# Kernel optimization log

Measured on AMD Instinct MI355X. Metric: run time of the kernel, lower is better.

## Reference

```python
import jax, jax.numpy as jnp
import numpy as np

H = W = 64
ALPHA = 1.0
BETA = 100.0
LIMB_PAIRS = np.array([[0,1],[1,2],[2,3],[0,4],[4,5],[5,6],[0,7],[7,8],[8,9],[9,10],
                       [8,11],[11,12],[12,13],[8,14],[14,15],[15,16]])
P0 = LIMB_PAIRS[:, 0]
P1 = LIMB_PAIRS[:, 1]
_last = {}
for _l, _j in enumerate(P0):
    _last[int(_j)] = _l
J0 = np.array(list(_last.keys()))   # unique proximal joints
L0 = np.array(list(_last.values())) # last limb writing to each joint


def make_kernel(h, w, alpha):
    # replicates: coords = stack(meshgrid(arange(2h-1), arange(2w-1))).transpose(1,2) (h==w)
    ii, jj = jnp.meshgrid(jnp.arange(2 * h - 1), jnp.arange(2 * w - 1), indexing='ij')
    ker = jnp.stack([h - jj, w - ii], axis=0).astype(jnp.float32)  # (2, 2h-1, 2w-1)
    dist = jnp.linalg.norm(ker, axis=0, keepdims=True)
    dist = dist.at[0, h, w].set(1.0)
    return ker / dist ** (1.0 + alpha)


def corr_full(x, k):
    # x: (N, Cin, h, w); k: (Cout, Cin, 2h-1, 2w-1); 'same' correlation with pad h-1/w-1
    h, w = x.shape[-2:]
    return jax.lax.conv_general_dilated(x, k, (1, 1), ((h - 1, h - 1), (w - 1, w - 1)))


def heatmap_std(x, di=False):
    axes = (3, 4, 5) if di else (3, 4)
    return jnp.std(x, axis=axes, keepdims=True, ddof=1)


def heatmap_normalize(x, std, di=False):
    return x * std / (heatmap_std(x, di) + 1e-6)


def l2norm(v, axis):
    return v / jnp.maximum(jnp.linalg.norm(v, axis=axis, keepdims=True), 1e-12)


def soft_argmax(hm, beta):
    # hm: ... x h x w -> ... x 2 with (row_coord, col_coord) as in the torch code
    h, w = hm.shape[-2:]
    p = jax.nn.softmax(hm.reshape(hm.shape[:-2] + (-1,)) * beta, axis=-1).reshape(hm.shape)
    rows = jnp.arange(h, dtype=p.dtype)[:, None]
    cols = jnp.arange(w, dtype=p.dtype)[None, :]
    norm = p.sum((-2, -1))
    kp_x = (p * rows).sum((-2, -1)) / norm
    kp_y = (p * cols).sum((-2, -1)) / norm
    return jnp.stack((kp_x, kp_y), axis=-1)


def scale_pts(pts, image_shape, h, w):
    return jnp.stack((pts[..., 0] * image_shape[1] / w,
                      pts[..., 1] * image_shape[0] / h), axis=-1)


def cofix_forward(heatmaps, fields, Ps, Rs, Cs, image_shape, confs, vth1, vth2, pth1, pth2):
    bs, nv, nL, _, h, w = fields.shape
    nJ = heatmaps.shape[2]
    K = make_kernel(h, w, ALPHA)  # (2, 2h-1, 2w-1)

    heatmaps = heatmaps - jnp.mean(heatmaps, axis=(3, 4), keepdims=True)
    std_hm = heatmap_std(heatmaps, di=False)
    std_df = heatmap_std(fields, di=True)

    Hs = heatmaps[:, :, P1] - heatmaps[:, :, P0]  # (bs, nv, nL, h, w)
    # conv3d(kernel1, flipped Hs) == 'same' correlation of Hs with spatially-reversed K
    k1 = K[:, ::-1, ::-1][:, None]  # (2, 1, 2h-1, 2w-1)
    convs = corr_full(Hs.reshape(-1, 1, h, w), k1).reshape(bs, nv, nL, 2, h, w)

    coef = jax.nn.relu(jnp.sum(convs * fields[..., :2, :, :], axis=3, keepdims=True))
    fields_new = fields * coef

    fnorm = jnp.linalg.norm(fields, axis=3, keepdims=True)
    lvecs = l2norm(jnp.sum(fnorm * fields, axis=(4, 5)), axis=3)
    lpts = scale_pts(soft_argmax(fnorm[:, :, :, 0], BETA), image_shape, h, w)

    fnorm_new = jnp.linalg.norm(fields_new, axis=3, keepdims=True)
    lvecs_new = l2norm(jnp.sum(fnorm_new * fields_new, axis=(4, 5)), axis=3)
    lpts_new = scale_pts(soft_argmax(fnorm_new[:, :, :, 0], BETA), image_shape, h, w)

    # original code computes vec_selection(...) then overwrites: delta[:] = 0
    delta = jnp.zeros((bs, nv, nL, 1), dtype=heatmaps.dtype)
    comb_v = delta * lvecs_new + (1 - delta) * lvecs
    comb_p = delta * lpts_new + (1 - delta) * lpts

    d6 = delta[..., None, None]
    fields_c = heatmap_normalize(fields * (1 - d6) + fields_new * d6, std_df, di=True)

    # conv2d(kernel2, fields) then output spatial flip == 'same' correlation with K
    k2 = K[None]  # (1, 2, 2h-1, 2w-1)
    fds2jts = corr_full(fields_c[..., :2, :, :].reshape(-1, 2, h, w), k2)
    fds2jts = fds2jts.reshape(bs, nv, nL, h, w)
    prox_ = jax.nn.relu(-fds2jts)
    dist_ = jax.nn.relu(fds2jts)

    hms_new = heatmaps.at[:, :, J0].set(heatmaps[:, :, J0] * prox_[:, :, L0])
    hms_new = hms_new.at[:, :, P1].set(hms_new[:, :, P1] * dist_)
    hms_new = heatmap_normalize(hms_new, std_hm, di=False)

    kps = scale_pts(soft_argmax(heatmaps, BETA), image_shape, h, w)[..., None]
    kps_new = scale_pts(soft_argmax(hms_new, BETA), image_shape, h, w)[..., None]
    kps_new = jnp.where(jnp.isnan(kps_new), kps, kps_new)

    # sed_selection (reconstructed): keep refined kps where joint conf is high and
    # the refinement displacement is small.
    confs_j = confs[:, :, nL:]
    disp = jnp.linalg.norm((kps_new - kps)[..., 0], axis=-1)  # (bs, nv, nJ)
    sel = ((confs_j > pth1) & (disp < pth2)).astype(kps.dtype)[..., None, None]
    kps_combined = sel * kps_new + (1 - sel) * kps

    return kps_combined, comb_v, comb_p, fields_new, hms_new


def setup_inputs() -> dict:
    key = jax.random.key(0)
    ks = jax.random.split(key, 6)
    bs, nv, nJ, nL = 4, 4, 17, 16
    return {
        'heatmaps': jax.random.uniform(ks[0], (bs, nv, nJ, H, W), jnp.float32),
        'fields': jax.random.normal(ks[1], (bs, nv, nL, 3, H, W), jnp.float32),
        'Ps': jax.random.normal(ks[2], (bs, nv, 3, 4), jnp.float32),
        'Rs': jax.random.normal(ks[3], (bs, nv, 3, 3), jnp.float32),
        'Cs': jax.random.normal(ks[4], (bs, nv, 3, 1), jnp.float32),
        'image_shape': jnp.array([384, 384], jnp.int32),
        'confs': jax.random.uniform(ks[5], (bs, nv, nL + nJ), jnp.float32),
        'vth1': 0.5, 'vth2': 0.5, 'pth1': 0.1, 'pth2': 20.0,
    }


def reference(heatmaps, fields, Ps, Rs, Cs, image_shape, confs, vth1, vth2, pth1, pth2):
    return cofix_forward(heatmaps, fields, Ps, Rs, Cs, image_shape, confs,
                         vth1, vth2, pth1, pth2)
```

## Files before the change

### kernel.cpp

```cpp
#include <hip/hip_runtime.h>
#include <math.h>

#define TPB 1024
#define HTPB 256
#define NPIX 4096
#define NJ 17
#define NL 16
static constexpr float kBeta = 100.0f;

#define O_KPS 0
#define O_CV 544
#define O_CP 1312
#define O_FN 1824
#define O_HM 3147552
#define W_FDS 0
#define W_MEAN 1048576
#define W_STD 1048848
#define W_SF 1049120
#define W_W1 1049376
#define W_W2 1082144

__device__ __constant__ int c_P0[16] = {0,1,2,0,4,5,0,7,8,9,8,11,12,8,14,15};
__device__ __constant__ int c_P1[16] = {1,2,3,4,5,6,7,8,9,10,11,12,13,14,15,16};
__device__ __constant__ int c_proxL[17] = {6,1,2,-1,4,5,-1,7,13,9,-1,11,12,-1,14,15,-1};
__device__ __constant__ int c_distL[17] = {-1,0,1,2,3,4,5,6,7,8,9,10,11,12,13,14,15};

using cplx = float2;
__device__ inline cplx cadd(cplx a, cplx b){ return {a.x+b.x, a.y+b.y}; }
__device__ inline cplx csub(cplx a, cplx b){ return {a.x-b.x, a.y-b.y}; }
__device__ inline cplx cmul(cplx a, cplx w){ return {a.x*w.x - a.y*w.y, a.x*w.y + a.y*w.x}; }
__device__ inline cplx cmulc(cplx a, cplx w){ return {a.x*w.x + a.y*w.y, a.y*w.x - a.x*w.y}; }

template<bool ROWS> __device__ inline int AD(int line, int p){
  return ROWS ? ((line<<7) | (p ^ (line & 15))) : ((p<<7) | (line ^ (p & 15)));
}

template<bool ROWS, bool INV, bool ZTOP, int NL_>
__device__ void pass_r2(cplx* S, const cplx* TW, int tid){
  constexpr int LOG2 = (NL_==128)?7:6;
  const int total = NL_*64;
  for (int idx = tid; idx < total; idx += TPB){
    const int line = idx & (NL_-1);
    const int b = idx >> LOG2;
    const cplx w = TW[b];
    const int a0 = AD<ROWS>(line, b);
    const int a1 = AD<ROWS>(line, b+64);
    if (ZTOP){
      const cplx u = S[a0];
      S[a1] = cmul(u, w);
    } else if (!INV){
      const cplx u = S[a0], v = S[a1];
      S[a0] = cadd(u,v);
      S[a1] = cmul(csub(u,v), w);
    } else {
      const cplx u = S[a0], t = cmulc(S[a1], w);
      S[a0] = cadd(u,t);
      S[a1] = csub(u,t);
    }
  }
  __syncthreads();
}

template<bool ROWS, bool INV, int Q, int NL_>
__device__ void pass_r4(cplx* S, const cplx* TW, int tid){
  constexpr int LOG2 = (NL_==128)?7:6;
  constexpr int LQ = (Q==16)?4:((Q==4)?2:0);
  constexpr int S_ = 32/Q;
  const int total = NL_*32;
  for (int idx = tid; idx < total; idx += TPB){
    const int line = idx & (NL_-1);
    const int b = idx >> LOG2;
    const int j = b & (Q-1);
    const int blk = b >> LQ;
    const int p0 = blk*(4*Q) + j;
    const int a0 = AD<ROWS>(line, p0);
    const int a1 = AD<ROWS>(line, p0+Q);
    const int a2 = AD<ROWS>(line, p0+2*Q);
    const int a3 = AD<ROWS>(line, p0+3*Q);
    const cplx x0=S[a0], x1=S[a1], x2=S[a2], x3=S[a3];
    if constexpr (!INV){
      const cplx a = cadd(x0,x2), bb = csub(x0,x2);
      const cplx c = cadd(x1,x3), d = csub(x1,x3);
      const cplx dp = {d.y, -d.x};
      if constexpr (Q==1){
        S[a0] = cadd(a,c);  S[a1] = csub(a,c);
        S[a2] = cadd(bb,dp); S[a3] = csub(bb,dp);
      } else {
        const cplx w1 = TW[j*S_], w2 = TW[2*j*S_], w3 = TW[3*j*S_];
        S[a0] = cadd(a,c);
        S[a1] = cmul(csub(a,c), w2);
        S[a2] = cmul(cadd(bb,dp), w1);
        S[a3] = cmul(csub(bb,dp), w3);
      }
    } else {
      cplx z1, z2, z3;
      if constexpr (Q==1){ z1 = x1; z2 = x2; z3 = x3; }
      else {
        const cplx w1 = TW[j*S_], w2 = TW[2*j*S_], w3 = TW[3*j*S_];
        z1 = cmulc(x1,w2); z2 = cmulc(x2,w1); z3 = cmulc(x3,w3);
      }
      const cplx A = cadd(x0,z1), C = csub(x0,z1);
      const cplx B = cadd(z2,z3), D = csub(z2,z3);
      const cplx iD = {-D.y, D.x};
      S[a0] = cadd(A,B);
      S[a1] = cadd(C,iD);
      S[a2] = csub(A,B);
      S[a3] = csub(C,iD);
    }
  }
  __syncthreads();
}

__device__ inline void tw_init(cplx* TW, int tid){
  if (tid < 96){
    float s, c;
    sincosf(-3.14159265358979323846f * (float)tid / 64.0f, &s, &c);
    TW[tid] = {c, s};
  }
  __syncthreads();
}

__device__ inline void fft2d_fwd_conv(cplx* S, const cplx* TW, int tid){
  pass_r2<true,  false, true, 64 >(S, TW, tid);
  pass_r4<true,  false, 16,   64 >(S, TW, tid);
  pass_r4<true,  false, 4,    64 >(S, TW, tid);
  pass_r4<true,  false, 1,    64 >(S, TW, tid);
  pass_r2<false, false, true, 128>(S, TW, tid);
  pass_r4<false, false, 16,   128>(S, TW, tid);
  pass_r4<false, false, 4,    128>(S, TW, tid);
  pass_r4<false, false, 1,    128>(S, TW, tid);
}
__device__ inline void fft2d_inv_conv(cplx* S, const cplx* TW, int tid){
  pass_r4<false, true, 1,    128>(S, TW, tid);
  pass_r4<false, true, 4,    128>(S, TW, tid);
  pass_r4<false, true, 16,   128>(S, TW, tid);
  pass_r2<false, true, false,128>(S, TW, tid);
  pass_r4<true,  true, 1,    64 >(S, TW, tid);
  pass_r4<true,  true, 4,    64 >(S, TW, tid);
  pass_r4<true,  true, 16,   64 >(S, TW, tid);
  pass_r2<true,  true, false,64 >(S, TW, tid);
}
__device__ inline void fft2d_fwd_full(cplx* S, const cplx* TW, int tid){
  pass_r2<true,  false, false,128>(S, TW, tid);
  pass_r4<true,  false, 16,   128>(S, TW, tid);
  pass_r4<true,  false, 4,    128>(S, TW, tid);
  pass_r4<true,  false, 1,    128>(S, TW, tid);
  pass_r2<false, false, false,128>(S, TW, tid);
  pass_r4<false, false, 16,   128>(S, TW, tid);
  pass_r4<false, false, 4,    128>(S, TW, tid);
  pass_r4<false, false, 1,    128>(S, TW, tid);
}

template<int N>
__device__ inline void reduce3n(float& a, float& b, float& c,
                                float* s0, float* s1, float* s2, int tid){
  s0[tid]=a; s1[tid]=b; s2[tid]=c; __syncthreads();
  for (int st = N/2; st; st >>= 1){
    if (tid < st){ s0[tid]+=s0[tid+st]; s1[tid]+=s1[tid+st]; s2[tid]+=s2[tid+st]; }
    __syncthreads();
  }
  a=s0[0]; b=s1[0]; c=s2[0]; __syncthreads();
}
template<int N>
__device__ inline float reduce_maxn(float v, float* s0, int tid){
  s0[tid]=v; __syncthreads();
  for (int st = N/2; st; st >>= 1){
    if (tid < st) s0[tid] = fmaxf(s0[tid], s0[tid+st]);
    __syncthreads();
  }
  const float r = s0[0]; __syncthreads();
  return r;
}

__global__ __launch_bounds__(TPB,1) void pre_kernel(const float* __restrict__ heat,
                                                    const float* __restrict__ fields,
                                                    const int* __restrict__ ishape,
                                                    float* __restrict__ mean_hm,
                                                    float* __restrict__ std_hm,
                                                    float* __restrict__ sf,
                                                    float* __restrict__ W1,
                                                    float* __restrict__ W2,
                                                    float* __restrict__ out){
  __shared__ cplx S[16384];
  __shared__ cplx TW[96];
  __shared__ float sA[TPB], sB[TPB], sC[TPB];
  const int tid = threadIdx.x;
  const int blk = blockIdx.x;
  if (blk < 272){
    const float* p = heat + (size_t)blk * NPIX;
    float s = 0.0f, s2 = 0.0f, d = 0.0f;
    for (int i = 0; i < 4; i++){
      const float x = p[tid + i*TPB];
      s += x; s2 += x*x;
    }
    reduce3n<TPB>(s, s2, d, sA, sB, sC, tid);
    if (tid == 0){
      const float mean = s / 4096.0f;
      const float var = (s2 - s*mean) / 4095.0f;
      mean_hm[blk] = mean;
      std_hm[blk] = sqrtf(fmaxf(var, 0.0f));
    }
  } else if (blk < 528){
    const int m = blk - 272;
    const float* f = fields + (size_t)m * 3 * NPIX;
    float s1 = 0.0f, s2 = 0.0f;
    float a0 = 0.0f, a1 = 0.0f, a2 = 0.0f;
    float fn[4];
    for (int i = 0; i < 4; i++){
      const int px = tid + i*TPB;
      const float f0 = f[px], f1 = f[NPIX+px], f2 = f[2*NPIX+px];
      s1 += f0+f1+f2; s2 += f0*f0+f1*f1+f2*f2;
      const float nn = sqrtf(f0*f0 + f1*f1 + f2*f2);
      fn[i] = nn;
      a0 += nn*f0; a1 += nn*f1; a2 += nn*f2;
    }
    {
      float t1 = s1, t2 = s2, t3 = 0.0f;
      reduce3n<TPB>(t1, t2, t3, sA, sB, sC, tid);
      if (tid == 0){
        const float var = (t2 - t1*t1/12288.0f) / 12287.0f;
        const float sd = sqrtf(fmaxf(var, 0.0f));
        sf[m] = sd / (sd + 1e-6f);
      }
    }
    reduce3n<TPB>(a0, a1, a2, sA, sB, sC, tid);
    float mx = fmaxf(fmaxf(fn[0],fn[1]), fmaxf(fn[2],fn[3]));
    mx = reduce_maxn<TPB>(mx, sA, tid);
    float Sm = 0.0f, Sx = 0.0f, Sy = 0.0f;
    for (int i = 0; i < 4; i++){
      const int px = tid + i*TPB;
      const float e = expf(kBeta * (fn[i] - mx));
      Sm += e; Sx += e * (float)(px>>6); Sy += e * (float)(px&63);
    }
    reduce3n<TPB>(Sm, Sx, Sy, sA, sB, sC, tid);
    if (tid == 0){
      float nrm = sqrtf(a0*a0 + a1*a1 + a2*a2);
      nrm = fmaxf(nrm, 1e-12f);
      out[O_CV + m*3 + 0] = a0/nrm;
      out[O_CV + m*3 + 1] = a1/nrm;
      out[O_CV + m*3 + 2] = a2/nrm;
      const float sxs = (float)ishape[1] / 64.0f;
      const float sys = (float)ishape[0] / 64.0f;
      out[O_CP + m*2 + 0] = Sx/Sm * sxs;
      out[O_CP + m*2 + 1] = Sy/Sm * sys;
    }
  } else {
    const int which = blk - 528;
    tw_init(TW, tid);
    for (int i = tid; i < 16384; i += TPB){
      const int r = i >> 7, c = i & 127;
      const int dy = (r < 64) ? r : r - 128;
      const int dx = (c < 64) ? c : c - 128;
      float a, b;
      if (which == 0){ a = 1.0f - (float)dy; b = 1.0f - (float)dx; }
      else           { a = 1.0f + (float)dy; b = 1.0f + (float)dx; }
      const float den = a*a + b*b;
      float vr = 0.0f, vi = 0.0f;
      if (r != 64 && c != 64 && den > 0.0f){
        const float inv = 1.0f/den;
        vr = a*inv; vi = -b*inv;
      }
      S[(r<<7) | (c ^ (r & 15))] = {vr, vi};
    }
    __syncthreads();
    fft2d_fwd_full(S, TW, tid);
    float2* Wo = (float2*)((which == 0) ? W1 : W2);
    const float scl = 1.0f / 16384.0f;
    for (int i = tid; i < 16384; i += TPB) Wo[i] = {S[i].x*scl, S[i].y*scl};
  }
}

__global__ __launch_bounds__(TPB,1) void conv_kernel(const float* __restrict__ heat,
                                                     const float* __restrict__ mean_hm,
                                                     const float* __restrict__ fields,
                                                     const float* __restrict__ sf,
                                                     const float* __restrict__ W1g,
                                                     const float* __restrict__ W2g,
                                                     float* __restrict__ out_fn,
                                                     float* __restrict__ fds){
  __shared__ cplx S[16384];
  __shared__ cplx TW[96];
  const int tid = threadIdx.x;
  const int n = blockIdx.x;
  tw_init(TW, tid);
  if (n < 256){
    const int bv = n >> 4, l = n & 15;
    const int j1 = bv*NJ + c_P1[l], j0 = bv*NJ + c_P0[l];
    const float* h1 = heat + (size_t)j1 * NPIX;
    const float* h0 = heat + (size_t)j0 * NPIX;
    const float dm = mean_hm[j1] - mean_hm[j0];
    for (int i = tid; i < NPIX; i += TPB){
      const int y = i >> 6, x = i & 63;
      S[(y<<7) | (x ^ (y & 15))] = {h1[i] - h0[i] - dm, 0.0f};
    }
    __syncthreads();
    fft2d_fwd_conv(S, TW, tid);
    const float2* Wg = (const float2*)W1g;
    for (int i = tid; i < 16384; i += TPB) S[i] = cmul(S[i], Wg[i]);
    __syncthreads();
    fft2d_inv_conv(S, TW, tid);
    const float* f = fields + (size_t)n * 3 * NPIX;
    float* o = out_fn + (size_t)n * 3 * NPIX;
    for (int i = tid; i < NPIX; i += TPB){
      const int y = i >> 6, x = i & 63;
      const cplx v = S[(y<<7) | (x ^ (y & 15))];
      const float c1 = v.x, c0 = -v.y;
      const float f0 = f[i], f1 = f[NPIX+i], f2 = f[2*NPIX+i];
      const float coef = fmaxf(0.0f, c0*f0 + c1*f1);
      o[i] = f0*coef; o[NPIX+i] = f1*coef; o[2*NPIX+i] = f2*coef;
    }
  } else {
    const int m = n - 256;
    const float* f = fields + (size_t)m * 3 * NPIX;
    for (int i = tid; i < NPIX; i += TPB){
      const int y = i >> 6, x = i & 63;
      S[(y<<7) | (x ^ (y & 15))] = {f[NPIX+i], f[i]};
    }
    __syncthreads();
    fft2d_fwd_conv(S, TW, tid);
    const float2* Wg = (const float2*)W2g;
    for (int i = tid; i < 16384; i += TPB) S[i] = cmul(S[i], Wg[i]);
    __syncthreads();
    fft2d_inv_conv(S, TW, tid);
    const float s = sf[m];
    float* o = fds + (size_t)m * NPIX;
    for (int i = tid; i < NPIX; i += TPB){
      const int y = i >> 6, x = i & 63;
      o[i] = S[(y<<7) | (x ^ (y & 15))].x * s;
    }
  }
}

__global__ __launch_bounds__(HTPB) void hms_kernel(const float* __restrict__ heat,
                                                   const float* __restrict__ mean_hm,
                                                   const float* __restrict__ std_hm,
                                                   const float* __restrict__ fds,
                                                   const float* __restrict__ confs,
                                                   const int* __restrict__ ishape,
                                                   const float* __restrict__ pth1p,
                                                   const float* __restrict__ pth2p,
                                                   float* __restrict__ out){
  __shared__ float sA[HTPB], sB[HTPB], sC[HTPB];
  const int tid = threadIdx.x;
  const int idx = blockIdx.x;
  const int bv = idx / NJ, j = idx % NJ;
  const float* hp = heat + (size_t)idx * NPIX;
  const float mh = mean_hm[idx];
  const int pl = c_proxL[j], dl = c_distL[j];
  const float* fp = (pl >= 0) ? fds + (size_t)(bv*NL + pl) * NPIX : nullptr;
  const float* fd = (dl >= 0) ? fds + (size_t)(bv*NL + dl) * NPIX : nullptr;
  float ho[16], hn[16];
  float s = 0.0f, s2 = 0.0f, dummy = 0.0f;
  for (int i = 0; i < 16; i++){
    const int px = tid + i*HTPB;
    const float h = hp[px] - mh;
    ho[i] = h;
    float m = h;
    if (pl >= 0) m *= fmaxf(0.0f, -fp[px]);
    if (dl >= 0) m *= fmaxf(0.0f, fd[px]);
    hn[i] = m;
    s += m; s2 += m*m;
  }
  reduce3n<HTPB>(s, s2, dummy, sA, sB, sC, tid);
  const float var = (s2 - s*s/4096.0f) / 4095.0f;
  const float sdn = sqrtf(fmaxf(var, 0.0f));
  const float scale = std_hm[idx] / (sdn + 1e-6f);
  float* ohm = out + O_HM + (size_t)idx * NPIX;
  for (int i = 0; i < 16; i++){
    hn[i] *= scale;
    ohm[tid + i*HTPB] = hn[i];
  }
  float mo = -1e30f, mn = -1e30f;
  for (int i = 0; i < 16; i++){ mo = fmaxf(mo, ho[i]); mn = fmaxf(mn, hn[i]); }
  mo = reduce_maxn<HTPB>(mo, sA, tid);
  mn = reduce_maxn<HTPB>(mn, sA, tid);
  float So = 0.0f, Sxo = 0.0f, Syo = 0.0f;
  float Sn = 0.0f, Sxn = 0.0f, Syn = 0.0f;
  for (int i = 0; i < 16; i++){
    const int px = tid + i*HTPB;
    const float y = (float)(px >> 6), x = (float)(px & 63);
    const float eo = expf(kBeta * (ho[i] - mo));
    So += eo; Sxo += eo*y; Syo += eo*x;
    const float en = expf(kBeta * (hn[i] - mn));
    Sn += en; Sxn += en*y; Syn += en*x;
  }
  reduce3n<HTPB>(So, Sxo, Syo, sA, sB, sC, tid);
  reduce3n<HTPB>(Sn, Sxn, Syn, sA, sB, sC, tid);
  if (tid == 0){
    const float sxs = (float)ishape[1] / 64.0f;
    const float sys = (float)ishape[0] / 64.0f;
    const float kxo = Sxo/So * sxs, kyo = Syo/So * sys;
    float kxn = Sxn/Sn * sxs, kyn = Syn/Sn * sys;
    if (kxn != kxn) kxn = kxo;
    if (kyn != kyn) kyn = kyo;
    const float ddx = kxn - kxo, ddy = kyn - kyo;
    const float disp = sqrtf(ddx*ddx + ddy*ddy);
    const float conf = confs[bv*(NL+NJ) + NL + j];
    const bool sel = (conf > pth1p[0]) && (disp < pth2p[0]);
    out[O_KPS + idx*2 + 0] = sel ? kxn : kxo;
    out[O_KPS + idx*2 + 1] = sel ? kyn : kyo;
  }
}

extern "C" void kernel_launch(void* const* d_in, const int* in_sizes, int n_in,
                              void* d_out, int out_size, void* d_ws, size_t ws_size,
                              hipStream_t stream) {
  const float* heat   = (const float*)d_in[0];
  const float* fields = (const float*)d_in[1];
  const int*   ishape = (const int*)d_in[5];
  const float* confs  = (const float*)d_in[6];
  const float* pth1   = (const float*)d_in[9];
  const float* pth2   = (const float*)d_in[10];
  float* out = (float*)d_out;
  float* ws = (float*)d_ws;
  float* fds     = ws + W_FDS;
  float* mean_hm = ws + W_MEAN;
  float* std_hm  = ws + W_STD;
  float* sf      = ws + W_SF;
  float* W1      = ws + W_W1;
  float* W2      = ws + W_W2;

  hipLaunchKernelGGL(pre_kernel, dim3(530), dim3(TPB), 0, stream,
                     heat, fields, ishape, mean_hm, std_hm, sf, W1, W2, out);
  hipLaunchKernelGGL(conv_kernel, dim3(512), dim3(TPB), 0, stream,
                     heat, mean_hm, fields, sf, W1, W2, out + O_FN, fds);
  hipLaunchKernelGGL(hms_kernel, dim3(272), dim3(HTPB), 0, stream,
                     heat, mean_hm, std_hm, fds, confs, ishape, pth1, pth2, out);
}
```

Measured before the change: 174.3 us.

## Replace radix-2/4 shared-memory FFT passes with register radix-8x16 decomposition

Rewrites the 128x128 2D FFT convolution so each thread loads a column or row chunk into registers and runs radix-8 then radix-16 butterflies. This cuts the number of shared-memory passes and __syncthreads barriers from eight to about four per direction. The frequency-domain multiply is fused into the middle column stage, and storage uses float4 pairs with an XOR swizzle. Loads and stores are vectorised, and launch bounds are relaxed. The cost is more register pressure from the 16-element register arrays, plus a risk of indexing or twiddle errors in the new decomposition.

```diff
diff --git a/kernel.cpp b/kernel.cpp
--- a/kernel.cpp
+++ b/kernel.cpp
@@ -7,6 +7,7 @@
 #define NJ 17
 #define NL 16
 static constexpr float kBeta = 100.0f;
+static constexpr float S2H = 0.70710678118654752f;
 
 #define O_KPS 0
 #define O_CV 544
@@ -31,124 +32,265 @@
 __device__ inline cplx cmul(cplx a, cplx w){ return {a.x*w.x - a.y*w.y, a.x*w.y + a.y*w.x}; }
 __device__ inline cplx cmulc(cplx a, cplx w){ return {a.x*w.x + a.y*w.y, a.y*w.x - a.x*w.y}; }
 
-template<bool ROWS> __device__ inline int AD(int line, int p){
-  return ROWS ? ((line<<7) | (p ^ (line & 15))) : ((p<<7) | (line ^ (p & 15)));
-}
-
-template<bool ROWS, bool INV, bool ZTOP, int NL_>
-__device__ void pass_r2(cplx* S, const cplx* TW, int tid){
-  constexpr int LOG2 = (NL_==128)?7:6;
-  const int total = NL_*64;
-  for (int idx = tid; idx < total; idx += TPB){
-    const int line = idx & (NL_-1);
-    const int b = idx >> LOG2;
-    const cplx w = TW[b];
-    const int a0 = AD<ROWS>(line, b);
-    const int a1 = AD<ROWS>(line, b+64);
-    if (ZTOP){
-      const cplx u = S[a0];
-      S[a1] = cmul(u, w);
-    } else if (!INV){
-      const cplx u = S[a0], v = S[a1];
-      S[a0] = cadd(u,v);
-      S[a1] = cmul(csub(u,v), w);
-    } else {
-      const cplx u = S[a0], t = cmulc(S[a1], w);
-      S[a0] = cadd(u,t);
-      S[a1] = csub(u,t);
-    }
-  }
-  __syncthreads();
-}
-
-template<bool ROWS, bool INV, int Q, int NL_>
-__device__ void pass_r4(cplx* S, const cplx* TW, int tid){
-  constexpr int LOG2 = (NL_==128)?7:6;
-  constexpr int LQ = (Q==16)?4:((Q==4)?2:0);
-  constexpr int S_ = 32/Q;
-  const int total = NL_*32;
-  for (int idx = tid; idx < total; idx += TPB){
-    const int line = idx & (NL_-1);
-    const int b = idx >> LOG2;
-    const int j = b & (Q-1);
-    const int blk = b >> LQ;
-    const int p0 = blk*(4*Q) + j;
-    const int a0 = AD<ROWS>(line, p0);
-    const int a1 = AD<ROWS>(line, p0+Q);
-    const int a2 = AD<ROWS>(line, p0+2*Q);
-    const int a3 = AD<ROWS>(line, p0+3*Q);
-    const cplx x0=S[a0], x1=S[a1], x2=S[a2], x3=S[a3];
-    if constexpr (!INV){
-      const cplx a = cadd(x0,x2), bb = csub(x0,x2);
-      const cplx c = cadd(x1,x3), d = csub(x1,x3);
-      const cplx dp = {d.y, -d.x};
-      if constexpr (Q==1){
-        S[a0] = cadd(a,c);  S[a1] = csub(a,c);
-        S[a2] = cadd(bb,dp); S[a3] = csub(bb,dp);
-      } else {
-        const cplx w1 = TW[j*S_], w2 = TW[2*j*S_], w3 = TW[3*j*S_];
-        S[a0] = cadd(a,c);
-        S[a1] = cmul(csub(a,c), w2);
-        S[a2] = cmul(cadd(bb,dp), w1);
-        S[a3] = cmul(csub(bb,dp), w3);
-      }
-    } else {
-      cplx z1, z2, z3;
-      if constexpr (Q==1){ z1 = x1; z2 = x2; z3 = x3; }
-      else {
-        const cplx w1 = TW[j*S_], w2 = TW[2*j*S_], w3 = TW[3*j*S_];
-        z1 = cmulc(x1,w2); z2 = cmulc(x2,w1); z3 = cmulc(x3,w3);
-      }
-      const cplx A = cadd(x0,z1), C = csub(x0,z1);
-      const cplx B = cadd(z2,z3), D = csub(z2,z3);
-      const cplx iD = {-D.y, D.x};
-      S[a0] = cadd(A,B);
-      S[a1] = cadd(C,iD);
-      S[a2] = csub(A,B);
-      S[a3] = csub(C,iD);
-    }
-  }
-  __syncthreads();
-}
-
-__device__ inline void tw_init(cplx* TW, int tid){
-  if (tid < 96){
-    float s, c;
-    sincosf(-3.14159265358979323846f * (float)tid / 64.0f, &s, &c);
-    TW[tid] = {c, s};
-  }
-  __syncthreads();
-}
-
-__device__ inline void fft2d_fwd_conv(cplx* S, const cplx* TW, int tid){
-  pass_r2<true,  false, true, 64 >(S, TW, tid);
-  pass_r4<true,  false, 16,   64 >(S, TW, tid);
-  pass_r4<true,  false, 4,    64 >(S, TW, tid);
-  pass_r4<true,  false, 1,    64 >(S, TW, tid);
-  pass_r2<false, false, true, 128>(S, TW, tid);
-  pass_r4<false, false, 16,   128>(S, TW, tid);
-  pass_r4<false, false, 4,    128>(S, TW, tid);
-  pass_r4<false, false, 1,    128>(S, TW, tid);
-}
-__device__ inline void fft2d_inv_conv(cplx* S, const cplx* TW, int tid){
-  pass_r4<false, true, 1,    128>(S, TW, tid);
-  pass_r4<false, true, 4,    128>(S, TW, tid);
-  pass_r4<false, true, 16,   128>(S, TW, tid);
-  pass_r2<false, true, false,128>(S, TW, tid);
-  pass_r4<true,  true, 1,    64 >(S, TW, tid);
-  pass_r4<true,  true, 4,    64 >(S, TW, tid);
-  pass_r4<true,  true, 16,   64 >(S, TW, tid);
-  pass_r2<true,  true, false,64 >(S, TW, tid);
-}
-__device__ inline void fft2d_fwd_full(cplx* S, const cplx* TW, int tid){
-  pass_r2<true,  false, false,128>(S, TW, tid);
-  pass_r4<true,  false, 16,   128>(S, TW, tid);
-  pass_r4<true,  false, 4,    128>(S, TW, tid);
-  pass_r4<true,  false, 1,    128>(S, TW, tid);
-  pass_r2<false, false, false,128>(S, TW, tid);
-  pass_r4<false, false, 16,   128>(S, TW, tid);
-  pass_r4<false, false, 4,    128>(S, TW, tid);
-  pass_r4<false, false, 1,    128>(S, TW, tid);
+__device__ __constant__ float2 W128BR[8] = {
+  {1.f,0.f},
+  {0.98078528040323044913f,-0.19509032201612826785f},
+  {0.99518472667219688624f,-0.09801714032956060199f},
+  {0.95694033573220886494f,-0.29028467725446236764f},
+  {0.99879545620517239271f,-0.04906767432741801425f},
+  {0.97003125319454399260f,-0.24298017990326388995f},
+  {0.98917650996478097345f,-0.14673047445536175166f},
+  {0.94154406518302077841f,-0.33688985339222005069f}
+};
+__device__ __constant__ float2 W16BR[8] = {
+  {1.f,0.f},
+  {0.f,-1.f},
+  {0.70710678118654752440f,-0.70710678118654752440f},
+  {-0.70710678118654752440f,-0.70710678118654752440f},
+  {0.92387953251128675613f,-0.38268343236508977173f},
+  {-0.38268343236508977173f,-0.92387953251128675613f},
+  {0.38268343236508977173f,-0.92387953251128675613f},
+  {-0.92387953251128675613f,-0.38268343236508977173f}
+};
+
+__device__ inline void bf8_tail(cplx t0, cplx t1, cplx t2, cplx t3,
+                                cplx t4, cplx t5, cplx t6, cplx t7, cplx x[8]){
+  cplx u0=cadd(t0,t2), u2=csub(t0,t2);
+  cplx u1=cadd(t1,t3), d13=csub(t1,t3);
+  cplx u3={d13.y,-d13.x};
+  cplx u4=cadd(t4,t6), u6=csub(t4,t6);
+  cplx u5=cadd(t5,t7), d57=csub(t5,t7);
+  cplx u7={d57.y,-d57.x};
+  x[0]=cadd(u0,u1); x[1]=csub(u0,u1);
+  x[2]=cadd(u2,u3); x[3]=csub(u2,u3);
+  x[4]=cadd(u4,u5); x[5]=csub(u4,u5);
+  x[6]=cadd(u6,u7); x[7]=csub(u6,u7);
+}
+__device__ inline void bf8_fwd(cplx x[8]){
+  cplx t0=cadd(x[0],x[4]), d4=csub(x[0],x[4]);
+  cplx t1=cadd(x[1],x[5]), d5=csub(x[1],x[5]);
+  cplx t2=cadd(x[2],x[6]), d6=csub(x[2],x[6]);
+  cplx t3=cadd(x[3],x[7]), d7=csub(x[3],x[7]);
+  cplx t5={S2H*(d5.x+d5.y), S2H*(d5.y-d5.x)};
+  cplx t6={d6.y,-d6.x};
+  cplx t7={S2H*(d7.y-d7.x), -S2H*(d7.x+d7.y)};
+  bf8_tail(t0,t1,t2,t3,d4,t5,t6,t7,x);
+}
+__device__ inline void bf8_fwd_z(cplx x[8]){
+  cplx t5={S2H*(x[1].x+x[1].y), S2H*(x[1].y-x[1].x)};
+  cplx t6={x[2].y,-x[2].x};
+  cplx t7={S2H*(x[3].y-x[3].x), -S2H*(x[3].x+x[3].y)};
+  bf8_tail(x[0],x[1],x[2],x[3],x[0],t5,t6,t7,x);
+}
+__device__ inline void bf8_inv(cplx y[8]){
+  cplx u0=cadd(y[0],y[1]), u1=csub(y[0],y[1]);
+  cplx u2=cadd(y[2],y[3]), u3=csub(y[2],y[3]);
+  cplx u4=cadd(y[4],y[5]), u5=csub(y[4],y[5]);
+  cplx u6=cadd(y[6],y[7]), u7=csub(y[6],y[7]);
+  cplx t0=cadd(u0,u2), t2=csub(u0,u2);
+  cplx iu3={-u3.y,u3.x};
+  cplx t1=cadd(u1,iu3), t3=csub(u1,iu3);
+  cplx t4=cadd(u4,u6), t6=csub(u4,u6);
+  cplx iu7={-u7.y,u7.x};
+  cplx t5=cadd(u5,iu7), t7=csub(u5,iu7);
+  y[0]=cadd(t0,t4); y[4]=csub(t0,t4);
+  cplx w5={S2H*(t5.x-t5.y), S2H*(t5.x+t5.y)};
+  y[1]=cadd(t1,w5); y[5]=csub(t1,w5);
+  cplx w6={-t6.y,t6.x};
+  y[2]=cadd(t2,w6); y[6]=csub(t2,w6);
+  cplx w7={-S2H*(t7.x+t7.y), S2H*(t7.x-t7.y)};
+  y[3]=cadd(t3,w7); y[7]=csub(t3,w7);
+}
+
+__device__ inline void fft16_fwd(cplx z[16]){
+  cplx e[8], o[8];
+  #pragma unroll
+  for (int t=0;t<8;t++){ e[t]=z[2*t]; o[t]=z[2*t+1]; }
+  bf8_fwd(e); bf8_fwd(o);
+  #pragma unroll
+  for (int p=0;p<8;p++){
+    cplx vo = cmul(o[p], W16BR[p]);
+    z[2*p]   = cadd(e[p], vo);
+    z[2*p+1] = csub(e[p], vo);
+  }
+}
+__device__ inline void fft16_inv(cplx z[16]){
+  cplx e[8], o[8];
+  #pragma unroll
+  for (int p=0;p<8;p++){
+    cplx a=z[2*p], b=z[2*p+1];
+    e[p] = cadd(a,b);
+    o[p] = cmulc(csub(a,b), W16BR[p]);
+  }
+  bf8_inv(e); bf8_inv(o);
+  #pragma unroll
+  for (int t=0;t<8;t++){ z[2*t]=e[t]; z[2*t+1]=o[t]; }
+}
+
+__device__ inline void twchainA(const cplx* TW, int j, cplx A[8]){
+  cplx W1 = TW[j];
+  cplx W2 = cmul(W1,W1);
+  cplx W4 = cmul(W2,W2);
+  cplx W6 = cmul(W4,W2);
+  A[0] = {1.f,0.f}; A[1] = W4; A[2] = W2; A[3] = W6;
+  A[4] = W1; A[5] = cmul(W4,W1); A[6] = cmul(W2,W1); A[7] = cmul(W6,W1);
+}
+
+__device__ inline int PH(int y, int m){ return (y<<6) | ((m ^ ((y&7)*9)) & 63); }
+
+template<int NLINES, bool ZT>
+__device__ void row_s1_fwd(float4* S4, const cplx* TW, int tid){
+  if (tid < NLINES*8){
+    const int L = tid>>3, m = tid&7;
+    cplx xe[8], xo[8];
+    #pragma unroll
+    for (int t=0; t<(ZT?4:8); t++){
+      float4 v = S4[PH(L, m+8*t)];
+      xe[t]={v.x,v.y}; xo[t]={v.z,v.w};
+    }
+    if (ZT){ bf8_fwd_z(xe); bf8_fwd_z(xo); } else { bf8_fwd(xe); bf8_fwd(xo); }
+    cplx A[8]; twchainA(TW, 2*m, A);
+    #pragma unroll
+    for (int p=0;p<8;p++){
+      cplx B = cmul(A[p], W128BR[p]);
+      cplx ve = cmul(xe[p], A[p]);
+      cplx vo = cmul(xo[p], B);
+      S4[PH(L, m+8*p)] = {ve.x, ve.y, vo.x, vo.y};
+    }
+  }
+  __syncthreads();
+}
+__device__ void row_s1_inv(float4* S4, const cplx* TW, int tid){
+  if (tid < 512){
+    const int L = tid>>3, m = tid&7;
+    cplx xe[8], xo[8];
+    #pragma unroll
+    for (int p=0;p<8;p++){
+      float4 v = S4[PH(L, m+8*p)];
+      xe[p]={v.x,v.y}; xo[p]={v.z,v.w};
+    }
+    cplx A[8]; twchainA(TW, 2*m, A);
+    #pragma unroll
+    for (int p=0;p<8;p++){
+      cplx B = cmul(A[p], W128BR[p]);
+      xe[p] = cmulc(xe[p], A[p]);
+      xo[p] = cmulc(xo[p], B);
+    }
+    bf8_inv(xe); bf8_inv(xo);
+    #pragma unroll
+    for (int t=0;t<4;t++)
+      S4[PH(L, m+8*t)] = {xe[t].x, xe[t].y, xo[t].x, xo[t].y};
+  }
+  __syncthreads();
+}
+template<int NLINES>
+__device__ void row_s2_fwd(float4* S4, int tid){
+  if (tid < NLINES*8){
+    const int L = tid>>3, jb = tid&7;
+    cplx z[16];
+    #pragma unroll
+    for (int k=0;k<8;k++){
+      float4 v = S4[PH(L, jb*8+k)];
+      z[2*k]={v.x,v.y}; z[2*k+1]={v.z,v.w};
+    }
+    fft16_fwd(z);
+    #pragma unroll
+    for (int k=0;k<8;k++)
+      S4[PH(L, jb*8+k)] = {z[2*k].x, z[2*k].y, z[2*k+1].x, z[2*k+1].y};
+  }
+  __syncthreads();
+}
+__device__ void row_s2_inv(float4* S4, int tid){
+  if (tid < 512){
+    const int L = tid>>3, jb = tid&7;
+    cplx z[16];
+    #pragma unroll
+    for (int k=0;k<8;k++){
+      float4 v = S4[PH(L, jb*8+k)];
+      z[2*k]={v.x,v.y}; z[2*k+1]={v.z,v.w};
+    }
+    fft16_inv(z);
+    #pragma unroll
+    for (int k=0;k<8;k++)
+      S4[PH(L, jb*8+k)] = {z[2*k].x, z[2*k].y, z[2*k+1].x, z[2*k+1].y};
+  }
+  __syncthreads();
+}
+template<bool ZT>
+__device__ void col_s1_fwd(float4* S4, const cplx* TW, int tid){
+  const int cp = tid & 63, yj = tid >> 6;
+  const int sl = (cp ^ ((yj&7)*9)) & 63;
+  cplx xe[8], xo[8];
+  #pragma unroll
+  for (int t=0; t<(ZT?4:8); t++){
+    float4 v = S4[((yj+16*t)<<6) | sl];
+    xe[t]={v.x,v.y}; xo[t]={v.z,v.w};
+  }
+  if (ZT){ bf8_fwd_z(xe); bf8_fwd_z(xo); } else { bf8_fwd(xe); bf8_fwd(xo); }
+  cplx A[8]; twchainA(TW, yj, A);
+  #pragma unroll
+  for (int p=0;p<8;p++){
+    cplx ve = cmul(xe[p], A[p]);
+    cplx vo = cmul(xo[p], A[p]);
+    S4[((yj+16*p)<<6) | sl] = {ve.x, ve.y, vo.x, vo.y};
+  }
+  __syncthreads();
+}
+__device__ void col_s1_inv(float4* S4, const cplx* TW, int tid){
+  const int cp = tid & 63, yj = tid >> 6;
+  const int sl = (cp ^ ((yj&7)*9)) & 63;
+  cplx xe[8], xo[8];
+  #pragma unroll
+  for (int p=0;p<8;p++){
+    float4 v = S4[((yj+16*p)<<6) | sl];
+    xe[p]={v.x,v.y}; xo[p]={v.z,v.w};
+  }
+  cplx A[8]; twchainA(TW, yj, A);
+  #pragma unroll
+  for (int p=0;p<8;p++){
+    xe[p] = cmulc(xe[p], A[p]);
+    xo[p] = cmulc(xo[p], A[p]);
+  }
+  bf8_inv(xe); bf8_inv(xo);
+  #pragma unroll
+  for (int t=0;t<4;t++)
+    S4[((yj+16*t)<<6) | sl] = {xe[t].x, xe[t].y, xo[t].x, xo[t].y};
+  __syncthreads();
+}
+__device__ void col_s2_fused(float4* S4, const cplx* __restrict__ Wg, int tid){
+  cplx* Sc = (cplx*)S4;
+  const int c = tid & 127, r = tid >> 7;
+  const int ch = c & 1, cp = c >> 1;
+  int ad[16];
+  cplx z[16];
+  #pragma unroll
+  for (int i=0;i<16;i++){
+    const int y = 16*r + i;
+    ad[i] = ((((y<<6) | ((cp ^ ((y&7)*9)) & 63)) << 1) | ch);
+    z[i] = Sc[ad[i]];
+  }
+  fft16_fwd(z);
+  #pragma unroll
+  for (int i=0;i<16;i++) z[i] = cmul(z[i], Wg[(16*r+i)*128 + c]);
+  fft16_inv(z);
+  #pragma unroll
+  for (int i=0;i<16;i++) Sc[ad[i]] = z[i];
+  __syncthreads();
+}
+__device__ void col_s2_fwd_store(float4* S4, cplx* __restrict__ Wo, int tid){
+  cplx* Sc = (cplx*)S4;
+  const int c = tid & 127, r = tid >> 7;
+  const int ch = c & 1, cp = c >> 1;
+  cplx z[16];
+  #pragma unroll
+  for (int i=0;i<16;i++){
+    const int y = 16*r + i;
+    z[i] = Sc[(((y<<6) | ((cp ^ ((y&7)*9)) & 63)) << 1) | ch];
+  }
+  fft16_fwd(z);
+  const float scl = 1.0f / 16384.0f;
+  #pragma unroll
+  for (int i=0;i<16;i++) Wo[(16*r+i)*128 + c] = {z[i].x*scl, z[i].y*scl};
 }
 
 template<int N>
@@ -172,7 +314,19 @@
   return r;
 }
 
-__global__ __launch_bounds__(TPB,1) void pre_kernel(const float* __restrict__ heat,
+__device__ inline cplx wval(int r, int c, int which){
+  const int dy = (r<64)? r : r-128;
+  const int dx = (c<64)? c : c-128;
+  float a, b;
+  if (which==0){ a = 1.f-(float)dy; b = 1.f-(float)dx; }
+  else         { a = 1.f+(float)dy; b = 1.f+(float)dx; }
+  const float den = a*a + b*b;
+  if (r==64 || c==64 || den<=0.f) return {0.f,0.f};
+  const float inv = 1.f/den;
+  return {a*inv, -b*inv};
+}
+
+__global__ __launch_bounds__(TPB,4) void pre_kernel(const float* __restrict__ heat,
                                                     const float* __restrict__ fields,
                                                     const int* __restrict__ ishape,
                                                     float* __restrict__ mean_hm,
@@ -181,8 +335,8 @@
                                                     float* __restrict__ W1,
                                                     float* __restrict__ W2,
                                                     float* __restrict__ out){
-  __shared__ cplx S[16384];
-  __shared__ cplx TW[96];
+  __shared__ float4 S4[8192];
+  __shared__ cplx TW[128];
   __shared__ float sA[TPB], sB[TPB], sC[TPB];
   const int tid = threadIdx.x;
   const int blk = blockIdx.x;
@@ -246,31 +400,26 @@
     }
   } else {
     const int which = blk - 528;
-    tw_init(TW, tid);
-    for (int i = tid; i < 16384; i += TPB){
-      const int r = i >> 7, c = i & 127;
-      const int dy = (r < 64) ? r : r - 128;
-      const int dx = (c < 64) ? c : c - 128;
-      float a, b;
-      if (which == 0){ a = 1.0f - (float)dy; b = 1.0f - (float)dx; }
-      else           { a = 1.0f + (float)dy; b = 1.0f + (float)dx; }
-      const float den = a*a + b*b;
-      float vr = 0.0f, vi = 0.0f;
-      if (r != 64 && c != 64 && den > 0.0f){
-        const float inv = 1.0f/den;
-        vr = a*inv; vi = -b*inv;
-      }
-      S[(r<<7) | (c ^ (r & 15))] = {vr, vi};
+    if (tid < 128){
+      float s, c;
+      sincosf(-6.283185307179586f * (float)tid / 128.0f, &s, &c);
+      TW[tid] = {c, s};
+    }
+    for (int s = tid; s < 8192; s += TPB){
+      const int y = s>>6, m = s&63;
+      const cplx v0 = wval(y, 2*m, which);
+      const cplx v1 = wval(y, 2*m+1, which);
+      S4[PH(y, m)] = {v0.x, v0.y, v1.x, v1.y};
     }
     __syncthreads();
-    fft2d_fwd_full(S, TW, tid);
-    float2* Wo = (float2*)((which == 0) ? W1 : W2);
-    const float scl = 1.0f / 16384.0f;
-    for (int i = tid; i < 16384; i += TPB) Wo[i] = {S[i].x*scl, S[i].y*scl};
-  }
-}
-
-__global__ __launch_bounds__(TPB,1) void conv_kernel(const float* __restrict__ heat,
+    row_s1_fwd<128,false>(S4, TW, tid);
+    row_s2_fwd<128>(S4, tid);
+    col_s1_fwd<false>(S4, TW, tid);
+    col_s2_fwd_store(S4, (cplx*)((which==0)?W1:W2), tid);
+  }
+}
+
+__global__ __launch_bounds__(TPB,4) void conv_kernel(const float* __restrict__ heat,
                                                      const float* __restrict__ mean_hm,
                                                      const float* __restrict__ fields,
                                                      const float* __restrict__ sf,
@@ -278,55 +427,71 @@
                                                      const float* __restrict__ W2g,
                                                      float* __restrict__ out_fn,
                                                      float* __restrict__ fds){
-  __shared__ cplx S[16384];
-  __shared__ cplx TW[96];
+  __shared__ float4 S4[8192];
+  __shared__ cplx TW[128];
   const int tid = threadIdx.x;
   const int n = blockIdx.x;
-  tw_init(TW, tid);
-  if (n < 256){
+  const bool is1 = (n < 256);
+  const int m_img = is1 ? n : (n - 256);
+  if (tid < 128){
+    float s, c;
+    sincosf(-6.283185307179586f * (float)tid / 128.0f, &s, &c);
+    TW[tid] = {c, s};
+  }
+  const float* f = fields + (size_t)m_img * 3 * NPIX;
+  if (is1){
     const int bv = n >> 4, l = n & 15;
     const int j1 = bv*NJ + c_P1[l], j0 = bv*NJ + c_P0[l];
     const float* h1 = heat + (size_t)j1 * NPIX;
     const float* h0 = heat + (size_t)j0 * NPIX;
     const float dm = mean_hm[j1] - mean_hm[j0];
-    for (int i = tid; i < NPIX; i += TPB){
-      const int y = i >> 6, x = i & 63;
-      S[(y<<7) | (x ^ (y & 15))] = {h1[i] - h0[i] - dm, 0.0f};
-    }
-    __syncthreads();
-    fft2d_fwd_conv(S, TW, tid);
-    const float2* Wg = (const float2*)W1g;
-    for (int i = tid; i < 16384; i += TPB) S[i] = cmul(S[i], Wg[i]);
-    __syncthreads();
-    fft2d_inv_conv(S, TW, tid);
-    const float* f = fields + (size_t)n * 3 * NPIX;
+    for (int s = tid; s < 2048; s += TPB){
+      const int y = s>>5, m = s&31;
+      const int i = (y<<6) + 2*m;
+      const float2 a = *(const float2*)(h1 + i);
+      const float2 b = *(const float2*)(h0 + i);
+      S4[PH(y, m)] = {a.x - b.x - dm, 0.f, a.y - b.y - dm, 0.f};
+    }
+  } else {
+    for (int s = tid; s < 2048; s += TPB){
+      const int y = s>>5, m = s&31;
+      const int i = (y<<6) + 2*m;
+      const float2 a = *(const float2*)(f + NPIX + i);
+      const float2 b = *(const float2*)(f + i);
+      S4[PH(y, m)] = {a.x, b.x, a.y, b.y};
+    }
+  }
+  __syncthreads();
+  row_s1_fwd<64,true>(S4, TW, tid);
+  row_s2_fwd<64>(S4, tid);
+  col_s1_fwd<true>(S4, TW, tid);
+  col_s2_fused(S4, (const cplx*)(is1 ? W1g : W2g), tid);
+  col_s1_inv(S4, TW, tid);
+  row_s2_inv(S4, tid);
+  row_s1_inv(S4, TW, tid);
+  if (is1){
     float* o = out_fn + (size_t)n * 3 * NPIX;
-    for (int i = tid; i < NPIX; i += TPB){
-      const int y = i >> 6, x = i & 63;
-      const cplx v = S[(y<<7) | (x ^ (y & 15))];
-      const float c1 = v.x, c0 = -v.y;
-      const float f0 = f[i], f1 = f[NPIX+i], f2 = f[2*NPIX+i];
-      const float coef = fmaxf(0.0f, c0*f0 + c1*f1);
-      o[i] = f0*coef; o[NPIX+i] = f1*coef; o[2*NPIX+i] = f2*coef;
+    for (int s = tid; s < 2048; s += TPB){
+      const int y = s>>5, m = s&31;
+      const int i = (y<<6) + 2*m;
+      const float4 v = S4[PH(y, m)];
+      const float2 f0 = *(const float2*)(f + i);
+      const float2 f1 = *(const float2*)(f + NPIX + i);
+      const float2 f2 = *(const float2*)(f + 2*NPIX + i);
+      const float cA = fmaxf(0.f, (-v.y)*f0.x + v.x*f1.x);
+      const float cB = fmaxf(0.f, (-v.w)*f0.y + v.z*f1.y);
+      *(float2*)(o + i)          = {f0.x*cA, f0.y*cB};
+      *(float2*)(o + NPIX + i)   = {f1.x*cA, f1.y*cB};
+      *(float2*)(o + 2*NPIX + i) = {f2.x*cA, f2.y*cB};
     }
   } else {
-    const int m = n - 256;
-    const float* f = fields + (size_t)m * 3 * NPIX;
-    for (int i = tid; i < NPIX; i += TPB){
-      const int y = i >> 6, x = i & 63;
-      S[(y<<7) | (x ^ (y & 15))] = {f[NPIX+i], f[i]};
-    }
-    __syncthreads();
-    fft2d_fwd_conv(S, TW, tid);
-    const float2* Wg = (const float2*)W2g;
-    for (int i = tid; i < 16384; i += TPB) S[i] = cmul(S[i], Wg[i]);
-    __syncthreads();
-    fft2d_inv_conv(S, TW, tid);
-    const float s = sf[m];
-    float* o = fds + (size_t)m * NPIX;
-    for (int i = tid; i < NPIX; i += TPB){
-      const int y = i >> 6, x = i & 63;
-      o[i] = S[(y<<7) | (x ^ (y & 15))].x * s;
+    const float sc = sf[m_img];
+    float* o = fds + (size_t)m_img * NPIX;
+    for (int s = tid; s < 2048; s += TPB){
+      const int y = s>>5, m = s&31;
+      const int i = (y<<6) + 2*m;
+      const float4 v = S4[PH(y, m)];
+      *(float2*)(o + i) = {v.x*sc, v.z*sc};
     }
   }
 }
```

Measured after the change: 159.8 us. 1.09x faster.
